# Kernel tuning notes

Hardware: AMD Instinct MI355X
Metric: run time of the kernel (lower is better)

The kernel has to match this reference:

```python
import jax, jax.numpy as jnp
import numpy as np

B, T, V, Q = 4, 4, 8192, 1024
C_IN, C_OUT, SD = 32, 16, 2
RF = 1.0 / 64.0
# max_neighbourhood implied by per-query quantile threshold (deterministic for
# continuous random distances): floor((V-1)*p) + 1
K_NEIGH = int(np.floor((V - 1) * RF)) + 1  # = 128
EPS = 1e-8
TEMP = 1.0
RFF_STD = 6.0


def setup_inputs() -> dict:
    key = jax.random.key(0)
    ks = jax.random.split(key, 12)
    return {
        "x": jax.random.normal(ks[0], (B, T, V, C_IN), jnp.float32),
        "pos": jax.random.uniform(ks[1], (V, SD), dtype=jnp.float32),
        "query_pos": jax.random.uniform(ks[2], (Q, SD), dtype=jnp.float32),
        "qmod_w": jax.random.uniform(ks[3], (Q, 32), dtype=jnp.float32),
        "qmod_off": jnp.zeros((Q, 32), jnp.float32),
        "W_lin": jax.random.normal(ks[4], (C_IN, C_IN), jnp.float32) / np.sqrt(C_IN).astype(np.float32),
        "b_lin": jnp.zeros((C_IN,), jnp.float32),
        "B_rff": RFF_STD * jax.random.normal(ks[5], (SD, 16), jnp.float32),
        "W1": jax.random.normal(ks[6], (32, 32), jnp.float32) / np.sqrt(32).astype(np.float32),
        "b1": jnp.zeros((32,), jnp.float32),
        "W2": jax.random.normal(ks[7], (32, C_IN * C_OUT), jnp.float32) / np.sqrt(32).astype(np.float32),
        "filt": jax.random.uniform(ks[8], (C_IN * C_OUT,), dtype=jnp.float32,
                                    minval=-np.sqrt(3.0 / C_IN), maxval=np.sqrt(3.0 / C_IN)),
        "bias_out": jnp.zeros((C_OUT,), jnp.float32),
        "Wm1": jax.random.normal(ks[9], (C_OUT, 4 * C_OUT), jnp.float32) / np.sqrt(C_OUT).astype(np.float32),
        "bm1": jnp.zeros((4 * C_OUT,), jnp.float32),
        "Wm2": jax.random.normal(ks[10], (4 * C_OUT, C_OUT), jnp.float32) / np.sqrt(4 * C_OUT).astype(np.float32),
        "bm2": jnp.zeros((C_OUT,), jnp.float32),
    }


def _gelu(x):
    return jax.nn.gelu(x, approximate=False)  # torch F.gelu default (erf)


def reference(x, pos, query_pos, qmod_w, qmod_off, W_lin, b_lin, B_rff,
              W1, b1, W2, filt, bias_out, Wm1, bm1, Wm2, bm2):
    # pairwise displacements, periodic wrap on unit torus
    d = query_pos[:, None, :] - pos[None, :, :]              # (Q,V,SD)
    d = (d + 0.5) % 1.0 - 0.5
    e = jnp.sum(d * d, axis=-1)                              # (Q,V) squared dist
    # nearest-K neighborhood (K = static max_neighbourhood from quantile mask)
    neg_e, ind = jax.lax.top_k(-e, K_NEIGH)                  # (Q,K)
    dist = jnp.take_along_axis(d, ind[:, :, None], axis=1)   # (Q,K,SD)
    edist = (-neg_e)[..., None]                              # (Q,K,1)
    edist = edist - jnp.min(edist, axis=-2, keepdims=True)
    edist = edist / (jnp.max(edist, axis=-2, keepdims=True) + EPS)
    k_dist = jax.nn.softmax(-edist / TEMP, axis=-2)          # (Q,K,1)
    # random Fourier features of displacements
    proj = (2.0 * jnp.pi) * (dist @ B_rff)                   # (Q,K,16)
    rff = jnp.concatenate([jnp.sin(proj), jnp.cos(proj)], axis=-1)  # (Q,K,32)
    # per-query modulated MLP kernel generation
    h = _gelu((rff @ W1 + b1) * qmod_w[:, None, :] + qmod_off[:, None, :])
    ker = (h @ W2 + filt) * k_dist                           # (Q,K,C_IN*C_OUT)
    ker = ker.reshape(Q, K_NEIGH, C_IN, C_OUT)
    # point features
    xl = x @ W_lin + b_lin                                   # (B,T,V,C_IN)
    xg = jnp.take(xl, ind, axis=2)                           # (B,T,Q,K,C_IN) gather
    y = jnp.einsum('qkcd,btqkc->btqd', ker, xg)              # (B,T,Q,C_OUT)
    y = _gelu(y + bias_out)
    y = (_gelu(y @ Wm1 + bm1) @ Wm2 + bm2) + y               # residual MLP
    return y, query_pos
```

## Files before the change

### kernel.cpp

```cpp
#include <hip/hip_runtime.h>
#include <math.h>
#include <stdint.h>

#define V_PTS 8192
#define NQ    1024
#define TWO_PI 6.283185307179586f
#define INV_SQRT2 0.70710678118654752f

typedef float floatx4 __attribute__((ext_vector_type(4)));
typedef short bf16x8 __attribute__((ext_vector_type(8)));
typedef _Float16 h16x2 __attribute__((ext_vector_type(2)));

union FragU { uint32_t u[4]; bf16x8 s; };
union WU { uint32_t u; h16x2 h; };

__device__ __forceinline__ float gelu_erf(float a) {
  return 0.5f * a * (1.0f + erff(a * INV_SQRT2));
}
__device__ __forceinline__ void gload_lds16(const void* g, void* l) {
  __builtin_amdgcn_global_load_lds(
      (const __attribute__((address_space(1))) void*)g,
      (__attribute__((address_space(3))) void*)l, 16, 0, 0);
}
__device__ __forceinline__ uint32_t pack_split(float f) {
  const uint32_t fu = __float_as_uint(f);
  const float lf = f - __uint_as_float(fu & 0xFFFF0000u);
  return __builtin_amdgcn_perm(fu, __float_as_uint(lf), 0x07060302u);
}
__device__ __forceinline__ void buildfrag(const uint4& w01, const uint4& w23,
                                          FragU& Fh, FragU& Fl) {
  const uint32_t w[8] = {w01.x, w01.y, w01.z, w01.w, w23.x, w23.y, w23.z, w23.w};
#pragma unroll
  for (int t = 0; t < 4; ++t) {
    Fh.u[t] = __builtin_amdgcn_perm(w[2 * t + 1], w[2 * t], 0x07060302u);
    Fl.u[t] = __builtin_amdgcn_perm(w[2 * t + 1], w[2 * t], 0x05040100u);
  }
}
#if __has_builtin(__builtin_amdgcn_fdot2)
#define FDOT2(G, W, ACC) ACC = __builtin_amdgcn_fdot2(G, W, ACC, false)
#else
#define FDOT2(G, W, ACC) ACC += (float)(G.x) * (float)(W.x) + (float)(G.y) * (float)(W.y)
#endif

__global__ __launch_bounds__(256) void prep_kernel(const float* __restrict__ Wl,
                                                   const float* __restrict__ bl,
                                                   const float* __restrict__ W2,
                                                   const float* __restrict__ filt,
                                                   float* __restrict__ W2p,
                                                   float* __restrict__ W2b) {
  __shared__ float sWl[1024];
  const int tid = threadIdx.x;
  for (int i = tid; i < 1024; i += 256) sWl[i] = Wl[i];
  __syncthreads();
  const int base = blockIdx.x * 528;
  for (int i = 0; i < 528; i += 256) {
    const int li = i + tid;
    if (li < 528) {
      const int idx = base + li;
      if (idx < 16896) {
        const int j = idx >> 9, r = idx & 511, cp = r >> 4, d = r & 15;
        const float* src = (j < 32) ? (W2 + (j << 9)) : filt;
        float acc = 0.0f;
#pragma unroll
        for (int c = 0; c < 32; ++c) acc = fmaf(sWl[cp * 32 + c], src[(c << 4) + d], acc);
        W2p[idx] = acc;
      }
    }
  }
  if (blockIdx.x == 0) {
    for (int idx = tid; idx < 528; idx += 256) {
      const int j = idx >> 4, d = idx & 15;
      const float* src = (j < 32) ? (W2 + (j << 9)) : filt;
      float acc = 0.0f;
#pragma unroll
      for (int c = 0; c < 32; ++c) acc = fmaf(bl[c], src[(c << 4) + d], acc);
      W2b[idx] = acc;
    }
  }
}

__global__ __launch_bounds__(256) void xsplit_kernel(const float* __restrict__ x,
                                                     const float* __restrict__ W2p,
                                                     uint32_t* __restrict__ xs,
                                                     uint32_t* __restrict__ W2pp) {
  const int bid = blockIdx.x, tid = threadIdx.x;
  if (bid < 1024) {
#pragma unroll
    for (int u = 0; u < 4; ++u) {
      const int i4 = (bid * 4 + u) * 256 + tid;
      const float4 f = ((const float4*)x)[i4];
      uint4 o;
      o.x = pack_split(f.x); o.y = pack_split(f.y);
      o.z = pack_split(f.z); o.w = pack_split(f.w);
      ((uint4*)xs)[i4] = o;
    }
  } else {
    const int idx = (bid - 1024) * 256 + tid;
    if (idx < 8704) {
      const int j2 = idx >> 9, r = idx & 511;
      const float w0 = W2p[(2 * j2) * 512 + r];
      const float w1 = (j2 < 16) ? W2p[(2 * j2 + 1) * 512 + r] : 0.0f;
      WU cv;
      cv.h.x = (_Float16)w0; cv.h.y = (_Float16)w1;
      W2pp[idx] = cv.u;
    }
  }
}

__global__ __launch_bounds__(256) void sel_kernel(
    const float* __restrict__ pos, const float* __restrict__ qpos,
    const float* __restrict__ qmw, const float* __restrict__ qmo,
    const float* __restrict__ Brff, const float* __restrict__ W1,
    const float* __restrict__ b1, const float* __restrict__ bout,
    const float* __restrict__ W2b,
    int* __restrict__ seli_ws, uint32_t* __restrict__ Hc_ws,
    uint32_t* __restrict__ kdp_ws, float* __restrict__ ybias_ws,
    float* __restrict__ out) {
  __shared__ float s_W1[1024];
  __shared__ __align__(16) float s_H2f[33 * 128];
  __shared__ int   s_seli[128];
  __shared__ float s_sele[128];
  __shared__ float s_kd[128];
  __shared__ float s_small[128];
  __shared__ int   s_redi[2][4];
  __shared__ unsigned s_redu[4];
  __shared__ int   s_wsum[4];
  __shared__ float s_red2[2];
  __shared__ float s_hsum[32];

  const int tid  = threadIdx.x;
  const int q    = blockIdx.x;
  const int lane = tid & 63;
  const int wv   = tid >> 6;

  for (int i = tid; i < 1024; i += 256) s_W1[i] = W1[i];
  if (tid < 32) {
    s_small[tid]      = Brff[tid];
    s_small[32 + tid] = b1[tid];
    s_small[64 + tid] = qmw[q * 32 + tid];
    s_small[96 + tid] = qmo[q * 32 + tid];
  }

  const float qx = qpos[2 * q], qy = qpos[2 * q + 1];

  unsigned u[32];
  unsigned umin = 0xFFFFFFFFu;
#pragma unroll
  for (int i = 0; i < 32; ++i) {
    const int v = i * 256 + tid;
    const float2 p = *(const float2*)(pos + 2 * v);
    float dx = qx - p.x + 0.5f; dx -= floorf(dx); dx -= 0.5f;
    float dy = qy - p.y + 0.5f; dy -= floorf(dy); dy -= 0.5f;
    const float e = dx * dx + dy * dy;
    u[i] = __float_as_uint(e);
    umin = min(umin, u[i]);
  }
#pragma unroll
  for (int off = 32; off > 0; off >>= 1) {
    unsigned o = (unsigned)__shfl_down((int)umin, off);
    umin = min(umin, o);
  }
  if (lane == 0) s_redu[wv] = umin;
  __syncthreads();
  const unsigned uminAll = min(min(s_redu[0], s_redu[1]), min(s_redu[2], s_redu[3]));

  unsigned lo = uminAll, hi = 0x3F000001u;
  int itp = 0;
  while (lo < hi) {
    const unsigned mid = lo + ((hi - lo) >> 1);
    int c = 0;
#pragma unroll
    for (int i = 0; i < 32; ++i)
      c += (int)__popcll(__ballot(u[i] <= mid));
    if (lane == 0) s_redi[itp][wv] = c;
    __syncthreads();
    const int tot = s_redi[itp][0] + s_redi[itp][1] + s_redi[itp][2] + s_redi[itp][3];
    itp ^= 1;
    if (tot >= 128) hi = mid; else lo = mid + 1;
  }
  const unsigned T = lo;

  int clt = 0, ceq = 0;
#pragma unroll
  for (int i = 0; i < 32; ++i) { clt += (u[i] < T) ? 1 : 0; ceq += (u[i] == T) ? 1 : 0; }
  int sv = clt | (ceq << 16);
#pragma unroll
  for (int off = 1; off < 64; off <<= 1) {
    const int n = __shfl_up(sv, off, 64);
    if (lane >= off) sv += n;
  }
  if (lane == 63) s_wsum[wv] = sv;
  __syncthreads();
  int add = 0;
#pragma unroll
  for (int w = 0; w < 4; ++w) add += (w < wv) ? s_wsum[w] : 0;
  const int incl   = sv + add;
  const int totAll = s_wsum[0] + s_wsum[1] + s_wsum[2] + s_wsum[3];
  const int totLt  = totAll & 0xFFFF;
  int plt = (incl & 0xFFFF) - clt;
  int peq = totLt + ((incl >> 16) - ceq);
#pragma unroll
  for (int i = 0; i < 32; ++i) {
    const int v = i * 256 + tid;
    if (u[i] < T)        { s_seli[plt] = v; s_sele[plt] = __uint_as_float(u[i]); ++plt; }
    else if (u[i] == T)  { if (peq < 128) { s_seli[peq] = v; s_sele[peq] = __uint_as_float(u[i]); } ++peq; }
  }
  __syncthreads();

  const float eminf = __uint_as_float(uminAll);
  const float emaxf = __uint_as_float(T);
  float wexp = 0.0f;
  if (tid < 128) {
    const float nrm = (s_sele[tid] - eminf) / ((emaxf - eminf) + 1e-8f);
    wexp = expf(-nrm);
  }
  if (wv < 2) {
    float ws = wexp;
#pragma unroll
    for (int m = 1; m < 64; m <<= 1) ws += __shfl_xor(ws, m, 64);
    if (lane == 0) s_red2[wv] = ws;
  }
  __syncthreads();
  const float wsum = s_red2[0] + s_red2[1];
  if (tid < 128) s_kd[tid] = wexp / wsum;
  __syncthreads();

  {
    const int k = tid >> 1, hh = tid & 1;
    const int v = s_seli[k];
    const float2 p = *(const float2*)(pos + 2 * v);
    float dx = qx - p.x + 0.5f; dx -= floorf(dx); dx -= 0.5f;
    float dy = qy - p.y + 0.5f; dy -= floorf(dy); dy -= 0.5f;
    float sn[16], cs[16];
#pragma unroll
    for (int i = 0; i < 16; ++i) {
      const float pr = TWO_PI * (dx * s_small[i] + dy * s_small[16 + i]);
      sn[i] = sinf(pr); cs[i] = cosf(pr);
    }
    const float kdv = s_kd[k];
#pragma unroll
    for (int jj = 0; jj < 16; ++jj) {
      const int j = hh * 16 + jj;
      float s = s_small[32 + j];
#pragma unroll
      for (int r = 0; r < 16; ++r) s = fmaf(sn[r], s_W1[r * 32 + j], s);
#pragma unroll
      for (int r = 0; r < 16; ++r) s = fmaf(cs[r], s_W1[(16 + r) * 32 + j], s);
      const float a = s * s_small[64 + j] + s_small[96 + j];
      s_H2f[j * 128 + k] = kdv * gelu_erf(a);
    }
    if (hh == 0) s_H2f[32 * 128 + k] = kdv;
  }
  __syncthreads();

  if (tid < 128) seli_ws[q * 128 + tid] = s_seli[tid];
  for (int idx = tid; idx < 4096; idx += 256) {
    const int ch = idx >> 10, j = (idx >> 5) & 31, p5 = idx & 31;
    const int k = ch * 32 + (p5 ^ ((j & 7) << 2));
    Hc_ws[(size_t)q * 4096 + idx] = pack_split(s_H2f[j * 128 + k]);
  }
  if (tid < 128) kdp_ws[q * 128 + tid] = pack_split(s_H2f[32 * 128 + tid]);
  {
    const int j = tid >> 3, m = tid & 7;
    float s = 0.0f;
#pragma unroll
    for (int i = 0; i < 16; ++i) s += s_H2f[j * 128 + m + i * 8];
    s += __shfl_xor(s, 1, 64); s += __shfl_xor(s, 2, 64); s += __shfl_xor(s, 4, 64);
    if (m == 0) s_hsum[j] = s;
  }
  __syncthreads();
  if (tid < 16) {
    float b = bout[tid] + W2b[32 * 16 + tid];
#pragma unroll
    for (int j = 0; j < 32; ++j) b = fmaf(s_hsum[j], W2b[j * 16 + tid], b);
    ybias_ws[q * 16 + tid] = b;
  }
  if (tid < 2) out[16 * NQ * 16 + q * 2 + tid] = qpos[q * 2 + tid];
}

__global__ __launch_bounds__(256) void main_kernel(
    const uint32_t* __restrict__ xs, const int* __restrict__ seli_ws,
    const uint32_t* __restrict__ Hc, const uint32_t* __restrict__ kdp,
    const float* __restrict__ ybias_ws, const uint32_t* __restrict__ W2pp,
    const float* __restrict__ Wm1, const float* __restrict__ bm1,
    const float* __restrict__ Wm2, const float* __restrict__ bm2,
    float* __restrict__ out) {
  __shared__ __align__(16) uint32_t s_X[2][4096];
  __shared__ __align__(16) uint32_t s_H[4096];
  __shared__ __align__(16) uint32_t s_kdp[128];
  __shared__ float s_ybias[16];
  __shared__ float s_part[4][4][16];
  __shared__ float s_y[64];
  __shared__ float s_z[256];

  const int tid  = threadIdx.x;
  const int lane = tid & 63;
  const int wv   = tid >> 6;
  const int q    = blockIdx.x >> 2;
  const int sub  = blockIdx.x & 3;

  const int grp = lane >> 4, m16 = lane & 15;
  const int gq   = (lane & 31) ^ (wv << 2);
  const int rsel = lane >> 5;
  const uint32_t* xcol = xs + ((size_t)(sub * 4 + (gq >> 3)) * V_PTS) * 32 + (gq & 7) * 4;

  int vsel[4][4];
#pragma unroll
  for (int ch = 0; ch < 4; ++ch)
#pragma unroll
    for (int t = 0; t < 4; ++t)
      vsel[ch][t] = seli_ws[q * 128 + ch * 32 + wv * 8 + 2 * t + rsel];

  if (tid < 128) s_kdp[tid] = kdp[q * 128 + tid];
  if (tid >= 128 && tid < 144) s_ybias[tid - 128] = ybias_ws[q * 16 + tid - 128];

  const uint32_t* Hq = Hc + (size_t)q * 4096;
#pragma unroll
  for (int hc = 0; hc < 4; ++hc)
    gload_lds16(Hq + hc * 1024 + tid * 4, s_H + hc * 1024 + wv * 256);

#define STAGE(CH)                                                           \
  {                                                                         \
    uint32_t* dstb = &s_X[(CH) & 1][0];                                     \
    _Pragma("unroll") for (int t = 0; t < 4; ++t) {                         \
      gload_lds16(xcol + (size_t)vsel[(CH)][t] * 32,                        \
                  dstb + (wv * 8 + 2 * t) * 128);                           \
    }                                                                       \
  }

  STAGE(0);
  STAGE(1);
  asm volatile("s_waitcnt vmcnt(0) lgkmcnt(0)\n\ts_barrier" ::: "memory");

  const int rd0 = ((((wv * 8 + 0) + (m16 >> 2)) ^ (grp << 2)) << 2) + (m16 & 3);
  const int rd1 = ((((wv * 8 + 4) + (m16 >> 2)) ^ (grp << 2)) << 2) + (m16 & 3);

  floatx4 acc[3][2];
#pragma unroll
  for (int a = 0; a < 3; ++a)
#pragma unroll
    for (int b = 0; b < 2; ++b) acc[a][b] = (floatx4){0.f, 0.f, 0.f, 0.f};

#define KBODY(CH)                                                              \
  {                                                                            \
    FragU Ah0, Al0, Ah1, Al1, Ah2, Al2;                                        \
    {                                                                          \
      const int swz = (m16 & 7) << 2;                                          \
      const uint32_t* h0 = s_H + (CH) * 1024 + m16 * 32;                       \
      const uint32_t* h1 = s_H + (CH) * 1024 + (16 + m16) * 32;                \
      const uint4 a0 = *(const uint4*)(h0 + ((grp * 8) ^ swz));                \
      const uint4 a1 = *(const uint4*)(h0 + ((grp * 8 + 4) ^ swz));            \
      const uint4 b0 = *(const uint4*)(h1 + ((grp * 8) ^ swz));                \
      const uint4 b1 = *(const uint4*)(h1 + ((grp * 8 + 4) ^ swz));            \
      const uint4 c0 = *(const uint4*)(s_kdp + (CH) * 32 + grp * 8);           \
      const uint4 c1 = *(const uint4*)(s_kdp + (CH) * 32 + grp * 8 + 4);       \
      buildfrag(a0, a1, Ah0, Al0);                                             \
      buildfrag(b0, b1, Ah1, Al1);                                             \
      buildfrag(c0, c1, Ah2, Al2);                                             \
      if (m16 != 0) {                                                          \
        _Pragma("unroll") for (int t = 0; t < 4; ++t) {                        \
          Ah2.u[t] = 0; Al2.u[t] = 0;                                          \
        }                                                                      \
      }                                                                        \
    }                                                                          \
    const uint32_t* Xb = &s_X[(CH) & 1][0];                                    \
    _Pragma("unroll") for (int nt = 0; nt < 2; ++nt) {                         \
      const int rdo = nt ? rd1 : rd0;                                          \
      uint32_t w[8];                                                           \
      _Pragma("unroll") for (int i = 0; i < 8; ++i)                            \
        w[i] = Xb[(grp * 8 + i) * 128 + rdo];                                  \
      FragU Bh, Bl;                                                            \
      _Pragma("unroll") for (int t = 0; t < 4; ++t) {                          \
        Bh.u[t] = __builtin_amdgcn_perm(w[2 * t + 1], w[2 * t], 0x07060302u);  \
        Bl.u[t] = __builtin_amdgcn_perm(w[2 * t + 1], w[2 * t], 0x05040100u);  \
      }                                                                        \
      acc[0][nt] = __builtin_amdgcn_mfma_f32_16x16x32_bf16(Ah0.s, Bh.s, acc[0][nt], 0, 0, 0); \
      acc[0][nt] = __builtin_amdgcn_mfma_f32_16x16x32_bf16(Al0.s, Bh.s, acc[0][nt], 0, 0, 0); \
      acc[0][nt] = __builtin_amdgcn_mfma_f32_16x16x32_bf16(Ah0.s, Bl.s, acc[0][nt], 0, 0, 0); \
      acc[1][nt] = __builtin_amdgcn_mfma_f32_16x16x32_bf16(Ah1.s, Bh.s, acc[1][nt], 0, 0, 0); \
      acc[1][nt] = __builtin_amdgcn_mfma_f32_16x16x32_bf16(Al1.s, Bh.s, acc[1][nt], 0, 0, 0); \
      acc[1][nt] = __builtin_amdgcn_mfma_f32_16x16x32_bf16(Ah1.s, Bl.s, acc[1][nt], 0, 0, 0); \
      acc[2][nt] = __builtin_amdgcn_mfma_f32_16x16x32_bf16(Ah2.s, Bh.s, acc[2][nt], 0, 0, 0); \
      acc[2][nt] = __builtin_amdgcn_mfma_f32_16x16x32_bf16(Al2.s, Bh.s, acc[2][nt], 0, 0, 0); \
      acc[2][nt] = __builtin_amdgcn_mfma_f32_16x16x32_bf16(Ah2.s, Bl.s, acc[2][nt], 0, 0, 0); \
    }                                                                          \
  }

  KBODY(0);
  asm volatile("s_waitcnt lgkmcnt(0)\n\ts_barrier" ::: "memory");
  STAGE(2);
  KBODY(1);
  asm volatile("s_waitcnt lgkmcnt(0)\n\ts_barrier" ::: "memory");
  STAGE(3);
  asm volatile("s_waitcnt vmcnt(4)\n\ts_barrier" ::: "memory");
  KBODY(2);
  asm volatile("s_waitcnt vmcnt(0)\n\ts_barrier" ::: "memory");
  KBODY(3);
#undef KBODY
#undef STAGE

  float yac[16];
#pragma unroll
  for (int e = 0; e < 16; ++e) yac[e] = 0.0f;
#pragma unroll
  for (int nt = 0; nt < 2; ++nt) {
    const int cp = nt * 16 + m16;
#pragma unroll
    for (int pp = 0; pp < 5; ++pp) {
      int j2; float g0, g1;
      if      (pp == 0) { j2 = grp * 2;         g0 = acc[0][nt][0]; g1 = acc[0][nt][1]; }
      else if (pp == 1) { j2 = grp * 2 + 1;     g0 = acc[0][nt][2]; g1 = acc[0][nt][3]; }
      else if (pp == 2) { j2 = 8 + grp * 2;     g0 = acc[1][nt][0]; g1 = acc[1][nt][1]; }
      else if (pp == 3) { j2 = 8 + grp * 2 + 1; g0 = acc[1][nt][2]; g1 = acc[1][nt][3]; }
      else              { j2 = 16;              g0 = acc[2][nt][0]; g1 = acc[2][nt][1]; }
      WU gw; gw.h.x = (_Float16)g0; gw.h.y = (_Float16)g1;
      const uint4* w4 = (const uint4*)(W2pp + ((j2 * 32 + cp) << 4));
#pragma unroll
      for (int e = 0; e < 4; ++e) {
        const uint4 ww = w4[e];
        WU wa, wb, wc, wd; wa.u = ww.x; wb.u = ww.y; wc.u = ww.z; wd.u = ww.w;
        FDOT2(gw.h, wa.h, yac[e * 4 + 0]);
        FDOT2(gw.h, wb.h, yac[e * 4 + 1]);
        FDOT2(gw.h, wc.h, yac[e * 4 + 2]);
        FDOT2(gw.h, wd.h, yac[e * 4 + 3]);
      }
    }
  }
#pragma unroll
  for (int m = 1; m <= 8; m <<= 1)
#pragma unroll
    for (int e = 0; e < 16; ++e) yac[e] += __shfl_xor(yac[e], m, 64);
  if (m16 == 0) {
#pragma unroll
    for (int e = 0; e < 16; ++e) s_part[wv][grp][e] = yac[e];
  }
  __syncthreads();

  if (tid < 64) {
    const int btl = tid >> 4, d = tid & 15;
    float y = s_part[btl][0][d] + s_part[btl][1][d] + s_part[btl][2][d] + s_part[btl][3][d];
    y += s_ybias[d];
    s_y[tid] = gelu_erf(y);
  }
  __syncthreads();
  {
    const int btl = tid >> 6, h = tid & 63;
    float s = bm1[h];
#pragma unroll
    for (int d2 = 0; d2 < 16; ++d2) s = fmaf(s_y[btl * 16 + d2], Wm1[d2 * 64 + h], s);
    s_z[btl * 64 + h] = gelu_erf(s);
  }
  __syncthreads();
  if (tid < 64) {
    const int btl = tid >> 4, d = tid & 15;
    float o = bm2[d];
#pragma unroll
    for (int h = 0; h < 64; ++h) o = fmaf(s_z[btl * 64 + h], Wm2[h * 16 + d], o);
    o += s_y[tid];
    out[((size_t)(sub * 4 + btl) * NQ + q) * 16 + d] = o;
  }
}

extern "C" void kernel_launch(void* const* d_in, const int* in_sizes, int n_in,
                              void* d_out, int out_size, void* d_ws, size_t ws_size,
                              hipStream_t stream) {
  const float* x    = (const float*)d_in[0];
  const float* pos  = (const float*)d_in[1];
  const float* qpos = (const float*)d_in[2];
  const float* qmw  = (const float*)d_in[3];
  const float* qmo  = (const float*)d_in[4];
  const float* Wl   = (const float*)d_in[5];
  const float* bl   = (const float*)d_in[6];
  const float* Brff = (const float*)d_in[7];
  const float* W1   = (const float*)d_in[8];
  const float* b1   = (const float*)d_in[9];
  const float* W2   = (const float*)d_in[10];
  const float* filt = (const float*)d_in[11];
  const float* bo   = (const float*)d_in[12];
  const float* Wm1  = (const float*)d_in[13];
  const float* bm1  = (const float*)d_in[14];
  const float* Wm2  = (const float*)d_in[15];
  const float* bm2  = (const float*)d_in[16];
  float* out = (float*)d_out;

  char* ws = (char*)d_ws;
  int*      seli_ws  = (int*)(ws + 0);
  uint32_t* Hc_ws    = (uint32_t*)(ws + 524288);
  uint32_t* kdp_ws   = (uint32_t*)(ws + 17301504);
  float*    ybias_ws = (float*)(ws + 17825792);
  float*    W2p_ws   = (float*)(ws + 17891328);
  float*    W2b_ws   = (float*)(ws + 17958912);
  uint32_t* W2pp_ws  = (uint32_t*)(ws + 17961024);
  uint32_t* xs_ws    = (uint32_t*)(ws + 17995840);

  hipLaunchKernelGGL(prep_kernel, dim3(32), dim3(256), 0, stream,
                     Wl, bl, W2, filt, W2p_ws, W2b_ws);
  hipLaunchKernelGGL(xsplit_kernel, dim3(1058), dim3(256), 0, stream,
                     x, W2p_ws, xs_ws, W2pp_ws);
  hipLaunchKernelGGL(sel_kernel, dim3(NQ), dim3(256), 0, stream,
                     pos, qpos, qmw, qmo, Brff, W1, b1, bo, W2b_ws,
                     seli_ws, Hc_ws, kdp_ws, ybias_ws, out);
  hipLaunchKernelGGL(main_kernel, dim3(4096), dim3(256), 0, stream,
                     xs_ws, seli_ws, Hc_ws, kdp_ws, ybias_ws, W2pp_ws,
                     Wm1, bm1, Wm2, bm2, out);
}
```

Baseline: 140.5 us.

## Merge prep kernels and load gathered X directly into registers

Fuses prep_kernel and xsplit_kernel into a single aux_kernel that builds the fp16-packed W2pp and the W2b bias directly, dropping one launch and the W2p intermediate buffer. In main_kernel, the LDS double-buffered staging of gathered x rows (global_load_lds plus barriers) is replaced by per-lane direct global loads into registers, double-buffered in registers. The selected indices now come from LDS. This removes LDS traffic and barriers but issues scattered 4-byte global loads instead of 16-byte LDS-DMA loads, which could hurt coalescing.

```diff
diff --git a/kernel.cpp b/kernel.cpp
--- a/kernel.cpp
+++ b/kernel.cpp
@@ -42,67 +42,55 @@
 #define FDOT2(G, W, ACC) ACC += (float)(G.x) * (float)(W.x) + (float)(G.y) * (float)(W.y)
 #endif
 
-__global__ __launch_bounds__(256) void prep_kernel(const float* __restrict__ Wl,
-                                                   const float* __restrict__ bl,
-                                                   const float* __restrict__ W2,
-                                                   const float* __restrict__ filt,
-                                                   float* __restrict__ W2p,
-                                                   float* __restrict__ W2b) {
-  __shared__ float sWl[1024];
-  const int tid = threadIdx.x;
-  for (int i = tid; i < 1024; i += 256) sWl[i] = Wl[i];
-  __syncthreads();
-  const int base = blockIdx.x * 528;
-  for (int i = 0; i < 528; i += 256) {
-    const int li = i + tid;
-    if (li < 528) {
-      const int idx = base + li;
-      if (idx < 16896) {
-        const int j = idx >> 9, r = idx & 511, cp = r >> 4, d = r & 15;
-        const float* src = (j < 32) ? (W2 + (j << 9)) : filt;
-        float acc = 0.0f;
-#pragma unroll
-        for (int c = 0; c < 32; ++c) acc = fmaf(sWl[cp * 32 + c], src[(c << 4) + d], acc);
-        W2p[idx] = acc;
-      }
-    }
-  }
-  if (blockIdx.x == 0) {
-    for (int idx = tid; idx < 528; idx += 256) {
-      const int j = idx >> 4, d = idx & 15;
-      const float* src = (j < 32) ? (W2 + (j << 9)) : filt;
-      float acc = 0.0f;
-#pragma unroll
-      for (int c = 0; c < 32; ++c) acc = fmaf(bl[c], src[(c << 4) + d], acc);
-      W2b[idx] = acc;
-    }
-  }
-}
-
-__global__ __launch_bounds__(256) void xsplit_kernel(const float* __restrict__ x,
-                                                     const float* __restrict__ W2p,
-                                                     uint32_t* __restrict__ xs,
-                                                     uint32_t* __restrict__ W2pp) {
+__global__ __launch_bounds__(256) void aux_kernel(
+    const float* __restrict__ x, const float* __restrict__ Wl,
+    const float* __restrict__ bl, const float* __restrict__ W2,
+    const float* __restrict__ filt,
+    uint32_t* __restrict__ xs, uint32_t* __restrict__ W2pp,
+    float* __restrict__ W2b) {
   const int bid = blockIdx.x, tid = threadIdx.x;
-  if (bid < 1024) {
+  if (bid >= 17) {
+    const int b = bid - 17;
 #pragma unroll
     for (int u = 0; u < 4; ++u) {
-      const int i4 = (bid * 4 + u) * 256 + tid;
+      const int i4 = (b * 4 + u) * 256 + tid;
       const float4 f = ((const float4*)x)[i4];
       uint4 o;
       o.x = pack_split(f.x); o.y = pack_split(f.y);
       o.z = pack_split(f.z); o.w = pack_split(f.w);
       ((uint4*)xs)[i4] = o;
     }
-  } else {
-    const int idx = (bid - 1024) * 256 + tid;
-    if (idx < 8704) {
-      const int j2 = idx >> 9, r = idx & 511;
-      const float w0 = W2p[(2 * j2) * 512 + r];
-      const float w1 = (j2 < 16) ? W2p[(2 * j2 + 1) * 512 + r] : 0.0f;
-      WU cv;
-      cv.h.x = (_Float16)w0; cv.h.y = (_Float16)w1;
-      W2pp[idx] = cv.u;
+    return;
+  }
+  __shared__ float sWl[1024];
+  for (int i = tid; i < 1024; i += 256) sWl[i] = Wl[i];
+  __syncthreads();
+  const int j2 = bid;
+  const float* srca = (j2 < 16) ? (W2 + (2 * j2) * 512) : filt;
+  const float* srcb = W2 + (2 * j2 + 1) * 512;
+#pragma unroll
+  for (int pass = 0; pass < 2; ++pass) {
+    const int r = pass * 256 + tid;
+    const int cp = r >> 4, d = r & 15;
+    float w0 = 0.0f, w1 = 0.0f;
+#pragma unroll
+    for (int c = 0; c < 32; ++c) {
+      const float wl = sWl[cp * 32 + c];
+      w0 = fmaf(wl, srca[(c << 4) + d], w0);
+      if (j2 < 16) w1 = fmaf(wl, srcb[(c << 4) + d], w1);
+    }
+    WU cv;
+    cv.h.x = (_Float16)w0; cv.h.y = (_Float16)w1;
+    W2pp[j2 * 512 + r] = cv.u;
+  }
+  if (tid < 32) {
+    const int j = 2 * j2 + (tid >> 4), d = tid & 15;
+    if (j <= 32) {
+      const float* src = (j < 32) ? (W2 + (j << 9)) : filt;
+      float acc = 0.0f;
+#pragma unroll
+      for (int c = 0; c < 32; ++c) acc = fmaf(bl[c], src[(c << 4) + d], acc);
+      W2b[j * 16 + d] = acc;
     }
   }
 }
@@ -285,9 +273,9 @@
     const float* __restrict__ Wm1, const float* __restrict__ bm1,
     const float* __restrict__ Wm2, const float* __restrict__ bm2,
     float* __restrict__ out) {
-  __shared__ __align__(16) uint32_t s_X[2][4096];
   __shared__ __align__(16) uint32_t s_H[4096];
   __shared__ __align__(16) uint32_t s_kdp[128];
+  __shared__ int   s_seli[128];
   __shared__ float s_ybias[16];
   __shared__ float s_part[4][4][16];
   __shared__ float s_y[64];
@@ -298,42 +286,20 @@
   const int wv   = tid >> 6;
   const int q    = blockIdx.x >> 2;
   const int sub  = blockIdx.x & 3;
-
-  const int grp = lane >> 4, m16 = lane & 15;
-  const int gq   = (lane & 31) ^ (wv << 2);
-  const int rsel = lane >> 5;
-  const uint32_t* xcol = xs + ((size_t)(sub * 4 + (gq >> 3)) * V_PTS) * 32 + (gq & 7) * 4;
-
-  int vsel[4][4];
-#pragma unroll
-  for (int ch = 0; ch < 4; ++ch)
-#pragma unroll
-    for (int t = 0; t < 4; ++t)
-      vsel[ch][t] = seli_ws[q * 128 + ch * 32 + wv * 8 + 2 * t + rsel];
-
-  if (tid < 128) s_kdp[tid] = kdp[q * 128 + tid];
-  if (tid >= 128 && tid < 144) s_ybias[tid - 128] = ybias_ws[q * 16 + tid - 128];
+  const int grp  = lane >> 4, m16 = lane & 15;
+
+  if (tid < 128) s_seli[tid] = seli_ws[q * 128 + tid];
+  if (tid >= 128 && tid < 256) s_kdp[tid - 128] = kdp[q * 128 + (tid - 128)];
+  if (tid < 16) s_ybias[tid] = ybias_ws[q * 16 + tid];
 
   const uint32_t* Hq = Hc + (size_t)q * 4096;
 #pragma unroll
   for (int hc = 0; hc < 4; ++hc)
     gload_lds16(Hq + hc * 1024 + tid * 4, s_H + hc * 1024 + wv * 256);
 
-#define STAGE(CH)                                                           \
-  {                                                                         \
-    uint32_t* dstb = &s_X[(CH) & 1][0];                                     \
-    _Pragma("unroll") for (int t = 0; t < 4; ++t) {                         \
-      gload_lds16(xcol + (size_t)vsel[(CH)][t] * 32,                        \
-                  dstb + (wv * 8 + 2 * t) * 128);                           \
-    }                                                                       \
-  }
-
-  STAGE(0);
-  STAGE(1);
   asm volatile("s_waitcnt vmcnt(0) lgkmcnt(0)\n\ts_barrier" ::: "memory");
 
-  const int rd0 = ((((wv * 8 + 0) + (m16 >> 2)) ^ (grp << 2)) << 2) + (m16 & 3);
-  const int rd1 = ((((wv * 8 + 4) + (m16 >> 2)) ^ (grp << 2)) << 2) + (m16 & 3);
+  const uint32_t* xbase = xs + ((size_t)(sub * 4 + wv) * V_PTS) * 32 + m16;
 
   floatx4 acc[3][2];
 #pragma unroll
@@ -341,7 +307,19 @@
 #pragma unroll
     for (int b = 0; b < 2; ++b) acc[a][b] = (floatx4){0.f, 0.f, 0.f, 0.f};
 
-#define KBODY(CH)                                                              \
+  int va[8], vb[8];
+  uint32_t ba[16], bb[16];
+
+#define LOADV(CH, V)                                                          \
+  _Pragma("unroll") for (int i = 0; i < 8; ++i)                               \
+    V[i] = s_seli[(CH) * 32 + grp * 8 + i];
+#define LOADB(V, B)                                                           \
+  _Pragma("unroll") for (int i = 0; i < 8; ++i) {                             \
+    const uint32_t* p = xbase + (size_t)V[i] * 32;                            \
+    B[i] = p[0]; B[8 + i] = p[16];                                            \
+  }
+
+#define KBODY(CH, B)                                                           \
   {                                                                            \
     FragU Ah0, Al0, Ah1, Al1, Ah2, Al2;                                        \
     {                                                                          \
@@ -363,16 +341,11 @@
         }                                                                      \
       }                                                                        \
     }                                                                          \
-    const uint32_t* Xb = &s_X[(CH) & 1][0];                                    \
     _Pragma("unroll") for (int nt = 0; nt < 2; ++nt) {                         \
-      const int rdo = nt ? rd1 : rd0;                                          \
-      uint32_t w[8];                                                           \
-      _Pragma("unroll") for (int i = 0; i < 8; ++i)                            \
-        w[i] = Xb[(grp * 8 + i) * 128 + rdo];                                  \
       FragU Bh, Bl;                                                            \
       _Pragma("unroll") for (int t = 0; t < 4; ++t) {                          \
-        Bh.u[t] = __builtin_amdgcn_perm(w[2 * t + 1], w[2 * t], 0x07060302u);  \
-        Bl.u[t] = __builtin_amdgcn_perm(w[2 * t + 1], w[2 * t], 0x05040100u);  \
+        Bh.u[t] = __builtin_amdgcn_perm(B[nt * 8 + 2 * t + 1], B[nt * 8 + 2 * t], 0x07060302u); \
+        Bl.u[t] = __builtin_amdgcn_perm(B[nt * 8 + 2 * t + 1], B[nt * 8 + 2 * t], 0x05040100u); \
       }                                                                        \
       acc[0][nt] = __builtin_amdgcn_mfma_f32_16x16x32_bf16(Ah0.s, Bh.s, acc[0][nt], 0, 0, 0); \
       acc[0][nt] = __builtin_amdgcn_mfma_f32_16x16x32_bf16(Al0.s, Bh.s, acc[0][nt], 0, 0, 0); \
@@ -386,18 +359,17 @@
     }                                                                          \
   }
 
-  KBODY(0);
-  asm volatile("s_waitcnt lgkmcnt(0)\n\ts_barrier" ::: "memory");
-  STAGE(2);
-  KBODY(1);
-  asm volatile("s_waitcnt lgkmcnt(0)\n\ts_barrier" ::: "memory");
-  STAGE(3);
-  asm volatile("s_waitcnt vmcnt(4)\n\ts_barrier" ::: "memory");
-  KBODY(2);
-  asm volatile("s_waitcnt vmcnt(0)\n\ts_barrier" ::: "memory");
-  KBODY(3);
+  LOADV(0, va); LOADB(va, ba);
+  LOADV(1, vb); LOADB(vb, bb);
+  KBODY(0, ba);
+  LOADV(2, va); LOADB(va, ba);
+  KBODY(1, bb);
+  LOADV(3, vb); LOADB(vb, bb);
+  KBODY(2, ba);
+  KBODY(3, bb);
 #undef KBODY
-#undef STAGE
+#undef LOADB
+#undef LOADV
 
   float yac[16];
 #pragma unroll
@@ -488,15 +460,12 @@
   uint32_t* Hc_ws    = (uint32_t*)(ws + 524288);
   uint32_t* kdp_ws   = (uint32_t*)(ws + 17301504);
   float*    ybias_ws = (float*)(ws + 17825792);
-  float*    W2p_ws   = (float*)(ws + 17891328);
-  float*    W2b_ws   = (float*)(ws + 17958912);
-  uint32_t* W2pp_ws  = (uint32_t*)(ws + 17961024);
-  uint32_t* xs_ws    = (uint32_t*)(ws + 17995840);
-
-  hipLaunchKernelGGL(prep_kernel, dim3(32), dim3(256), 0, stream,
-                     Wl, bl, W2, filt, W2p_ws, W2b_ws);
-  hipLaunchKernelGGL(xsplit_kernel, dim3(1058), dim3(256), 0, stream,
-                     x, W2p_ws, xs_ws, W2pp_ws);
+  float*    W2b_ws   = (float*)(ws + 17891328);
+  uint32_t* W2pp_ws  = (uint32_t*)(ws + 17893440);
+  uint32_t* xs_ws    = (uint32_t*)(ws + 17928256);
+
+  hipLaunchKernelGGL(aux_kernel, dim3(1041), dim3(256), 0, stream,
+                     x, Wl, bl, W2, filt, xs_ws, W2pp_ws, W2b_ws);
   hipLaunchKernelGGL(sel_kernel, dim3(NQ), dim3(256), 0, stream,
                      pos, qpos, qmw, qmo, Brff, W1, b1, bo, W2b_ws,
                      seli_ws, Hc_ws, kdp_ws, ybias_ws, out);
```

After: 136.5 us, median of 3. -2.8%, faster.
